# Optimization experiments

Hardware: AMD Instinct MI355X
Metric: run time of the kernel (lower is better)

The kernel has to match this reference:

```python
import jax, jax.numpy as jnp
import numpy as np

NUM_FREQUENCIES = 6  # K = 2F+1 = 13


def fourier_basis(times, num_frequencies):
    # times: [N] -> basis: [N, 2F+1] = [1, sin(2^j*pi*t), cos(2^j*pi*t)]
    freqs = (2.0 ** jnp.arange(num_frequencies, dtype=times.dtype)) * jnp.pi  # [F]
    ang = times[:, None] * freqs[None, :]  # [N, F]
    ones = jnp.ones_like(times)[:, None]
    return jnp.concatenate([ones, jnp.sin(ang), jnp.cos(ang)], axis=-1)  # [N, K]


def setup_inputs() -> dict:
    key = jax.random.key(0)
    k1, k2, k3 = jax.random.split(key, 3)
    N, num_videos, embedding_dim = 400000, 128, 64
    times = jax.random.uniform(k1, (N,), dtype=jnp.float32)
    video_ids = jax.random.randint(k2, (N,), 0, num_videos, dtype=jnp.int32)
    weights = jax.random.normal(k3, (num_videos, embedding_dim, 2 * NUM_FREQUENCIES + 1), dtype=jnp.float32)
    return {"times": times, "video_ids": video_ids, "weights": weights}


def reference(times, video_ids, weights):
    basis = fourier_basis(times, NUM_FREQUENCIES)          # [N, K]
    w = weights[video_ids]                                  # gather: [N, D, K]
    return jnp.einsum('nk,ndk->nd', basis, w)               # [N, D]
```

## Files before the change

### kernel.cpp

```cpp
#include <hip/hip_runtime.h>
#include <math.h>


#define V 128
#define D 64
#define K 13
#define CHUNK 1024
#define BS 256
#define PER (CHUNK / BS)
#define BST 16

__global__ __launch_bounds__(256, 2) void fused_kernel(
    const float* __restrict__ times, const int* __restrict__ ids,
    const float* __restrict__ weights, float* __restrict__ out, int n)
{
    __shared__ float basis[CHUNK * BST];
    __shared__ unsigned short list[CHUNK];
    __shared__ int cnt[V];
    __shared__ int start[V];
    __shared__ int cur[V];

    int tid = threadIdx.x;
    int base = blockIdx.x * CHUNK;

    if (tid < V) cnt[tid] = 0;
    __syncthreads();

    int myv[PER];
#pragma unroll
    for (int i = 0; i < PER; ++i) {
        int li = i * BS + tid;
        int g = base + li;
        myv[i] = -1;
        if (g < n) {
            float t = times[g];
            int v = ids[g];
            myv[i] = v;
            atomicAdd(&cnt[v], 1);
            float s, c;
            __sincosf(3.14159265358979323846f * t, &s, &c);
            float sa[6], ca[6];
            sa[0] = s; ca[0] = c;
#pragma unroll
            for (int j = 1; j < 6; ++j) {
                sa[j] = 2.0f * sa[j - 1] * ca[j - 1];
                ca[j] = 1.0f - 2.0f * sa[j - 1] * sa[j - 1];
            }
            float4* bp = (float4*)&basis[li * BST];
            bp[0] = make_float4(1.0f, sa[0], sa[1], sa[2]);
            bp[1] = make_float4(sa[3], sa[4], sa[5], ca[0]);
            bp[2] = make_float4(ca[1], ca[2], ca[3], ca[4]);
            basis[li * BST + 12] = ca[5];
        }
    }
    __syncthreads();

    if (tid < V) start[tid] = cnt[tid];
    __syncthreads();
    for (int off = 1; off < V; off <<= 1) {
        int val = 0;
        if (tid < V && tid >= off) val = start[tid - off];
        __syncthreads();
        if (tid < V) start[tid] += val;
        __syncthreads();
    }
    if (tid < V) { start[tid] -= cnt[tid]; cur[tid] = 0; }
    __syncthreads();

#pragma unroll
    for (int i = 0; i < PER; ++i) {
        if (myv[i] >= 0) {
            int r = atomicAdd(&cur[myv[i]], 1);
            list[start[myv[i]] + r] = (unsigned short)(i * BS + tid);
        }
    }
    __syncthreads();

    int wave = tid >> 6;
    int lane = tid & 63;
    for (int v = wave; v < V; v += 4) {
        int c = cnt[v];
        if (c == 0) continue;
        int s0 = start[v];
        const float* wp = weights + (v * D + lane) * K;
        float w0 = wp[0], w1 = wp[1], w2 = wp[2], w3 = wp[3];
        float w4 = wp[4], w5 = wp[5], w6 = wp[6], w7 = wp[7];
        float w8 = wp[8], w9 = wp[9], w10 = wp[10], w11 = wp[11], w12 = wp[12];
        for (int j = 0; j < c; ++j) {
            int li = list[s0 + j];
            const float4* bp = (const float4*)&basis[li * BST];
            float4 b0 = bp[0], b1 = bp[1], b2 = bp[2];
            float b12 = basis[li * BST + 12];
            float acc = ((b0.x * w0 + b0.y * w1) + (b0.z * w2 + b0.w * w3))
                      + ((b1.x * w4 + b1.y * w5) + (b1.z * w6 + b1.w * w7))
                      + (((b2.x * w8 + b2.y * w9) + (b2.z * w10 + b2.w * w11))
                         + b12 * w12);
            out[(long)(base + li) * D + lane] = acc;
        }
    }
}

extern "C" void kernel_launch(void* const* d_in, const int* in_sizes, int n_in,
                              void* d_out, int out_size, void* d_ws, size_t ws_size,
                              hipStream_t stream) {
    const float* times = (const float*)d_in[0];
    const int* ids = (const int*)d_in[1];
    const float* weights = (const float*)d_in[2];
    float* out = (float*)d_out;
    int n = in_sizes[0];

    int nblk = (n + CHUNK - 1) / CHUNK;
    fused_kernel<<<nblk, BS, 0, stream>>>(times, ids, weights, out, n);
}
```

Before: 153.3 us.

## Pack video id into sorted list and write float4 outputs per lane

Halves the chunk size and raises the occupancy hint. The sorted list now packs the local index together with the video id. Each wave splits its slice of the sorted list among four groups of 16 lanes, and each lane computes four output columns and stores them as a float4. This replaces the per-video wave loop with scalar stores, evening out load across waves and widening global stores. In exchange, each lane holds 52 weight registers and reloads weights whenever the video id changes, which adds register pressure and extra weight traffic.

```diff
diff --git a/kernel.cpp b/kernel.cpp
--- a/kernel.cpp
+++ b/kernel.cpp
@@ -5,12 +5,12 @@
 #define V 128
 #define D 64
 #define K 13
-#define CHUNK 1024
+#define CHUNK 512
 #define BS 256
 #define PER (CHUNK / BS)
 #define BST 16
 
-__global__ __launch_bounds__(256, 2) void fused_kernel(
+__global__ __launch_bounds__(256, 4) void fused_kernel(
     const float* __restrict__ times, const int* __restrict__ ids,
     const float* __restrict__ weights, float* __restrict__ out, int n)
 {
@@ -22,6 +22,7 @@
 
     int tid = threadIdx.x;
     int base = blockIdx.x * CHUNK;
+    int total = n - base; if (total > CHUNK) total = CHUNK;
 
     if (tid < V) cnt[tid] = 0;
     __syncthreads();
@@ -70,33 +71,51 @@
 #pragma unroll
     for (int i = 0; i < PER; ++i) {
         if (myv[i] >= 0) {
+            int li = i * BS + tid;
             int r = atomicAdd(&cur[myv[i]], 1);
-            list[start[myv[i]] + r] = (unsigned short)(i * BS + tid);
+            list[start[myv[i]] + r] = (unsigned short)((li << 7) | myv[i]);
         }
     }
     __syncthreads();
 
     int wave = tid >> 6;
     int lane = tid & 63;
-    for (int v = wave; v < V; v += 4) {
-        int c = cnt[v];
-        if (c == 0) continue;
-        int s0 = start[v];
-        const float* wp = weights + (v * D + lane) * K;
-        float w0 = wp[0], w1 = wp[1], w2 = wp[2], w3 = wp[3];
-        float w4 = wp[4], w5 = wp[5], w6 = wp[6], w7 = wp[7];
-        float w8 = wp[8], w9 = wp[9], w10 = wp[10], w11 = wp[11], w12 = wp[12];
-        for (int j = 0; j < c; ++j) {
-            int li = list[s0 + j];
-            const float4* bp = (const float4*)&basis[li * BST];
-            float4 b0 = bp[0], b1 = bp[1], b2 = bp[2];
-            float b12 = basis[li * BST + 12];
-            float acc = ((b0.x * w0 + b0.y * w1) + (b0.z * w2 + b0.w * w3))
-                      + ((b1.x * w4 + b1.y * w5) + (b1.z * w6 + b1.w * w7))
-                      + (((b2.x * w8 + b2.y * w9) + (b2.z * w10 + b2.w * w11))
-                         + b12 * w12);
-            out[(long)(base + li) * D + lane] = acc;
+    int n_sub = lane >> 4;
+    int dq = lane & 15;
+    int j0 = wave * (CHUNK / 4);
+    int j1 = (wave + 1) * (CHUNK / 4); if (j1 > total) j1 = total;
+
+    int vcur = -1;
+    float wf[52];
+    for (int j = j0; j < j1; j += 4) {
+        int jj = j + n_sub;
+        bool valid = (jj < j1);
+        unsigned int e = valid ? (unsigned int)list[jj] : 0u;
+        int li = (int)(e >> 7);
+        int v = (int)(e & 127u);
+        if (valid && v != vcur) {
+            vcur = v;
+            const float4* wp = (const float4*)(weights + (v * D + dq * 4) * K);
+#pragma unroll
+            for (int q = 0; q < 13; ++q) *((float4*)&wf[q * 4]) = wp[q];
         }
+        const float4* bp = (const float4*)&basis[li * BST];
+        float4 b0 = bp[0], b1 = bp[1], b2 = bp[2];
+        float bk12 = basis[li * BST + 12];
+        float bk[13] = { b0.x, b0.y, b0.z, b0.w, b1.x, b1.y, b1.z, b1.w,
+                         b2.x, b2.y, b2.z, b2.w, bk12 };
+        float4 acc;
+        float* ap = &acc.x;
+#pragma unroll
+        for (int dd = 0; dd < 4; ++dd) {
+            const float* w = &wf[dd * 13];
+            ap[dd] = ((bk[0] * w[0] + bk[1] * w[1]) + (bk[2] * w[2] + bk[3] * w[3]))
+                   + ((bk[4] * w[4] + bk[5] * w[5]) + (bk[6] * w[6] + bk[7] * w[7]))
+                   + (((bk[8] * w[8] + bk[9] * w[9]) + (bk[10] * w[10] + bk[11] * w[11]))
+                      + bk[12] * w[12]);
+        }
+        if (valid)
+            *(float4*)(out + (long)(base + li) * D + dq * 4) = acc;
     }
 }
 
```

After: 191.8 us. +25.1%, slower.

## Sort basis rows by video and split sorted rows evenly across waves

Applied to the files above, without the earlier changes.

Basis computation moves after the counting sort so each row's basis is written directly into its sorted slot, together with a packed output-index/video tag. Each wave then handles an equal contiguous slice of the sorted rows and reloads weights only when the video id changes. This replaces the old per-video loop over waves, which could leave waves unevenly loaded. The chunk is halved to 512 and occupancy raised to 4 blocks per SM to reduce LDS use and add waves, at the cost of more weight reloads across blocks.

```diff
diff --git a/kernel.cpp b/kernel.cpp
--- a/kernel.cpp
+++ b/kernel.cpp
@@ -5,52 +5,39 @@
 #define V 128
 #define D 64
 #define K 13
-#define CHUNK 1024
+#define CHUNK 512
 #define BS 256
 #define PER (CHUNK / BS)
 #define BST 16
 
-__global__ __launch_bounds__(256, 2) void fused_kernel(
+__global__ __launch_bounds__(256, 4) void fused_kernel(
     const float* __restrict__ times, const int* __restrict__ ids,
     const float* __restrict__ weights, float* __restrict__ out, int n)
 {
     __shared__ float basis[CHUNK * BST];
-    __shared__ unsigned short list[CHUNK];
+    __shared__ int oidx[CHUNK];
     __shared__ int cnt[V];
     __shared__ int start[V];
     __shared__ int cur[V];
 
     int tid = threadIdx.x;
     int base = blockIdx.x * CHUNK;
+    int total = n - base; if (total > CHUNK) total = CHUNK;
 
     if (tid < V) cnt[tid] = 0;
     __syncthreads();
 
+    float myt[PER];
     int myv[PER];
 #pragma unroll
     for (int i = 0; i < PER; ++i) {
-        int li = i * BS + tid;
-        int g = base + li;
+        int g = base + i * BS + tid;
         myv[i] = -1;
         if (g < n) {
-            float t = times[g];
+            myt[i] = times[g];
             int v = ids[g];
             myv[i] = v;
             atomicAdd(&cnt[v], 1);
-            float s, c;
-            __sincosf(3.14159265358979323846f * t, &s, &c);
-            float sa[6], ca[6];
-            sa[0] = s; ca[0] = c;
-#pragma unroll
-            for (int j = 1; j < 6; ++j) {
-                sa[j] = 2.0f * sa[j - 1] * ca[j - 1];
-                ca[j] = 1.0f - 2.0f * sa[j - 1] * sa[j - 1];
-            }
-            float4* bp = (float4*)&basis[li * BST];
-            bp[0] = make_float4(1.0f, sa[0], sa[1], sa[2]);
-            bp[1] = make_float4(sa[3], sa[4], sa[5], ca[0]);
-            bp[2] = make_float4(ca[1], ca[2], ca[3], ca[4]);
-            basis[li * BST + 12] = ca[5];
         }
     }
     __syncthreads();
@@ -70,33 +57,56 @@
 #pragma unroll
     for (int i = 0; i < PER; ++i) {
         if (myv[i] >= 0) {
-            int r = atomicAdd(&cur[myv[i]], 1);
-            list[start[myv[i]] + r] = (unsigned short)(i * BS + tid);
+            int v = myv[i];
+            float t = myt[i];
+            float s, c;
+            __sincosf(3.14159265358979323846f * t, &s, &c);
+            float sa[6], ca[6];
+            sa[0] = s; ca[0] = c;
+#pragma unroll
+            for (int j = 1; j < 6; ++j) {
+                sa[j] = 2.0f * sa[j - 1] * ca[j - 1];
+                ca[j] = 1.0f - 2.0f * sa[j - 1] * sa[j - 1];
+            }
+            int r = atomicAdd(&cur[v], 1);
+            int pos = start[v] + r;
+            float4* bp = (float4*)&basis[pos * BST];
+            bp[0] = make_float4(1.0f, sa[0], sa[1], sa[2]);
+            bp[1] = make_float4(sa[3], sa[4], sa[5], ca[0]);
+            bp[2] = make_float4(ca[1], ca[2], ca[3], ca[4]);
+            basis[pos * BST + 12] = ca[5];
+            oidx[pos] = ((base + i * BS + tid) << 7) | v;
         }
     }
     __syncthreads();
 
     int wave = tid >> 6;
     int lane = tid & 63;
-    for (int v = wave; v < V; v += 4) {
-        int c = cnt[v];
-        if (c == 0) continue;
-        int s0 = start[v];
-        const float* wp = weights + (v * D + lane) * K;
-        float w0 = wp[0], w1 = wp[1], w2 = wp[2], w3 = wp[3];
-        float w4 = wp[4], w5 = wp[5], w6 = wp[6], w7 = wp[7];
-        float w8 = wp[8], w9 = wp[9], w10 = wp[10], w11 = wp[11], w12 = wp[12];
-        for (int j = 0; j < c; ++j) {
-            int li = list[s0 + j];
-            const float4* bp = (const float4*)&basis[li * BST];
-            float4 b0 = bp[0], b1 = bp[1], b2 = bp[2];
-            float b12 = basis[li * BST + 12];
-            float acc = ((b0.x * w0 + b0.y * w1) + (b0.z * w2 + b0.w * w3))
-                      + ((b1.x * w4 + b1.y * w5) + (b1.z * w6 + b1.w * w7))
-                      + (((b2.x * w8 + b2.y * w9) + (b2.z * w10 + b2.w * w11))
-                         + b12 * w12);
-            out[(long)(base + li) * D + lane] = acc;
+    int j0 = wave * (CHUNK / 4);
+    int j1 = j0 + (CHUNK / 4); if (j1 > total) j1 = total;
+
+    int vcur = -1;
+    float w0, w1, w2, w3, w4, w5, w6, w7, w8, w9, w10, w11, w12;
+    w0=w1=w2=w3=w4=w5=w6=w7=w8=w9=w10=w11=w12 = 0.0f;
+#pragma unroll 2
+    for (int j = j0; j < j1; ++j) {
+        int e = oidx[j];
+        int v = e & 127;
+        const float4* bp = (const float4*)&basis[j * BST];
+        float4 b0 = bp[0], b1 = bp[1], b2 = bp[2];
+        float bk12 = basis[j * BST + 12];
+        if (v != vcur) {
+            vcur = v;
+            const float* wp = weights + (v * D + lane) * K;
+            w0 = wp[0];  w1 = wp[1];  w2 = wp[2];  w3 = wp[3];
+            w4 = wp[4];  w5 = wp[5];  w6 = wp[6];  w7 = wp[7];
+            w8 = wp[8];  w9 = wp[9];  w10 = wp[10]; w11 = wp[11]; w12 = wp[12];
         }
+        float acc = ((b0.x * w0 + b0.y * w1) + (b0.z * w2 + b0.w * w3))
+                  + ((b1.x * w4 + b1.y * w5) + (b1.z * w6 + b1.w * w7))
+                  + (((b2.x * w8 + b2.y * w9) + (b2.z * w10 + b2.w * w11))
+                     + bk12 * w12);
+        out[(long)(e >> 7) * D + lane] = acc;
     }
 }
 
```

New measurement: 146.6 us. -4.4%, faster.
